# Kernel optimization log

Hardware: AMD Instinct MI355X
Metric: run time of the kernel (lower is better)

The kernel has to match this reference:

```python
import jax, jax.numpy as jnp
import numpy as np

DIM = 1024
DIM_HEAD = 64
HEADS = 16
NUM_LATENTS = 64
INNER = DIM_HEAD * HEADS  # 1024


def setup_inputs() -> dict:
    key = jax.random.key(0)
    ks = jax.random.split(key, 6)
    b, m, n = 8, 4, 1024
    x = jax.random.normal(ks[0], (b, m, n, DIM), dtype=jnp.float32)
    latents = jax.random.normal(ks[1], (NUM_LATENTS, DIM), dtype=jnp.float32)
    # Linear weights stored as (in, out); no bias for q/kv, bias for out (matches nn.Linear defaults)
    Wq = jax.random.normal(ks[2], (DIM, INNER), dtype=jnp.float32) * (DIM ** -0.5)
    Wkv = jax.random.normal(ks[3], (DIM, INNER * 2), dtype=jnp.float32) * (DIM ** -0.5)
    Wout = jax.random.normal(ks[4], (INNER, DIM), dtype=jnp.float32) * (INNER ** -0.5)
    bout = jax.random.normal(ks[5], (DIM,), dtype=jnp.float32) * 0.01
    return {"x": x, "latents": latents, "Wq": Wq, "Wkv": Wkv, "Wout": Wout, "bout": bout}


def reference(x, latents, Wq, Wkv, Wout, bout):
    b, m, n, d = x.shape
    h, dh = HEADS, DIM_HEAD
    scale = dh ** -0.5

    # q from latents: [n_lat, inner] -> [h, i, dh]
    q = (latents @ Wq).reshape(NUM_LATENTS, h, dh).transpose(1, 0, 2) * scale

    # k, v from media tokens: [b, m, n, 2*inner] -> two [b, h, m, n, dh]
    kv = x @ Wkv
    k, v = jnp.split(kv, 2, axis=-1)
    k = k.reshape(b, m, n, h, dh).transpose(0, 3, 1, 2, 4)  # b h m n dh
    v = v.reshape(b, m, n, h, dh).transpose(0, 3, 1, 2, 4)

    # latent k, v: [n_lat, 2*inner] -> [h, n_lat, dh] broadcast to [b, h, m, n_lat, dh]
    lkv = latents @ Wkv
    lk, lv = jnp.split(lkv, 2, axis=-1)
    lk = jnp.broadcast_to(lk.reshape(NUM_LATENTS, h, dh).transpose(1, 0, 2)[None, :, None], (b, h, m, NUM_LATENTS, dh))
    lv = jnp.broadcast_to(lv.reshape(NUM_LATENTS, h, dh).transpose(1, 0, 2)[None, :, None], (b, h, m, NUM_LATENTS, dh))

    k = jnp.concatenate((k, lk), axis=-2)  # b h m (n + n_lat) dh
    v = jnp.concatenate((v, lv), axis=-2)

    sim = jnp.einsum('hid,bhmjd->bhmij', q, k)
    attn = jax.nn.softmax(sim, axis=-1)  # stable softmax (max-subtract internal)
    out = jnp.einsum('bhmij,bhmjd->bhmid', attn, v)  # b h m i dh
    out = out.transpose(0, 2, 3, 1, 4).reshape(b, m, NUM_LATENTS, h * dh)  # b m i inner
    return out @ Wout + bout
```

## Files before the change

kernel.cpp:

```cpp
#include <hip/hip_runtime.h>
#include <cstdint>

typedef __attribute__((ext_vector_type(8))) __bf16 bf16x8;
typedef __attribute__((ext_vector_type(4))) float f32x4;
typedef __attribute__((ext_vector_type(8))) unsigned short u16x8;
typedef __attribute__((ext_vector_type(4))) unsigned short u16x4;

__device__ __forceinline__ unsigned short f2bf(float f) {
    union { float f; unsigned u; } v; v.f = f;
    unsigned u = v.u;
    return (unsigned short)((u + 0x7FFFu + ((u >> 16) & 1u)) >> 16);
}

__device__ __forceinline__ void gload_lds16(const void* g, void* l) {
    auto gp = reinterpret_cast<__attribute__((address_space(1))) unsigned*>(
        reinterpret_cast<uintptr_t>(g));
    auto lp = reinterpret_cast<__attribute__((address_space(3))) unsigned*>(
        reinterpret_cast<uintptr_t>(l));
    __builtin_amdgcn_global_load_lds(gp, lp, 16, 0, 0);
}

__global__ __launch_bounds__(256) void prep(const float* __restrict__ x,
                                            const float* __restrict__ latents,
                                            const float* __restrict__ Wq,
                                            const float* __restrict__ Wkv,
                                            const float* __restrict__ Wout,
                                            unsigned short* __restrict__ xb,
                                            unsigned short* __restrict__ latb,
                                            unsigned short* __restrict__ wqkvt,
                                            unsigned short* __restrict__ wkvt,
                                            unsigned short* __restrict__ woutt) {
    int b = blockIdx.x, tid = threadIdx.x;
    if (b < 2048) {
        int idx = b * 256 + tid, stride = 2048 * 256;
        for (int i = idx; i < 8388608; i += stride) {
            float4 v = ((const float4*)x)[i];
            u16x4 o;
            o.x = f2bf(v.x); o.y = f2bf(v.y); o.z = f2bf(v.z); o.w = f2bf(v.w);
            ((u16x4*)xb)[i] = o;
        }
        return;
    }
    b -= 2048;
    if (b < 64) {
        int i = b * 256 + tid;
        float4 v = ((const float4*)latents)[i];
        u16x4 o;
        o.x = f2bf(v.x); o.y = f2bf(v.y); o.z = f2bf(v.z); o.w = f2bf(v.w);
        ((u16x4*)latb)[i] = o;
        return;
    }
    b -= 64;
    const float* in; unsigned short* out; int R, C, bx, by;
    if (b < 1024)      { in = Wq;   out = wqkvt; R = 1024; C = 1024; bx = b & 31; by = b >> 5; }
    else if (b < 3072) { int v = b - 1024; in = Wkv;  out = wkvt;  R = 1024; C = 2048; bx = v & 63; by = v >> 6; }
    else               { int v = b - 3072; in = Wout; out = woutt; R = 1024; C = 1024; bx = v & 31; by = v >> 5; }
    __shared__ float t[32][33];
    int c0 = bx * 32, r0 = by * 32;
    int tx = tid & 31, ty = tid >> 5;
    for (int i = ty; i < 32; i += 8)
        t[i][tx] = in[(size_t)(r0 + i) * C + c0 + tx];
    __syncthreads();
    for (int i = ty; i < 32; i += 8)
        out[(size_t)(c0 + i) * R + r0 + tx] = f2bf(t[tx][i]);
}

__device__ __forceinline__ void gemm128p_body(const unsigned short* __restrict__ A,
                                              const unsigned short* __restrict__ Bt,
                                              void* __restrict__ C,
                                              const float* __restrict__ bias,
                                              unsigned short* __restrict__ vT,
                                              int M, int N, int K, float scale, int split,
                                              int c_f32, int vstart,
                                              int tid, int bid, int nwg,
                                              unsigned short* ldsbuf) {
#define LDSP(bi, half) (ldsbuf + ((bi) * 2 + (half)) * 4096)
    int ntx = N >> 7;
    int swz = bid;
    if ((nwg & 7) == 0) { int cpx = nwg >> 3; swz = (bid & 7) * cpx + (bid >> 3); }
    int m0 = (swz / ntx) << 7, n0 = (swz % ntx) << 7;
    int lane = tid & 63, w = tid >> 6;
    int wm = w >> 1, wn = w & 1;
    int lr = lane & 15, lg = lane >> 4;
    int gq = lg ^ ((lr >> 1) & 3);
    int nkt = K >> 5;

    int arow = tid >> 2;
    int sgl = (tid & 3) ^ ((arow >> 1) & 3);
    int ra0 = m0 + arow;      if (ra0 > M - 1) ra0 = M - 1;
    int ra1 = m0 + 64 + arow; if (ra1 > M - 1) ra1 = M - 1;
    const unsigned short* a0 = A + (size_t)ra0 * K + (sgl << 3);
    const unsigned short* a1 = A + (size_t)ra1 * K + (sgl << 3);
    const unsigned short* b0 = Bt + (size_t)(n0 + arow) * K + (sgl << 3);
    const unsigned short* b1 = Bt + (size_t)(n0 + 64 + arow) * K + (sgl << 3);

    f32x4 acc[4][4] = {};

#define ST_A128(bi, kt) do { \
        gload_lds16(a0 + ((kt) << 5), LDSP(bi, 0) + (w << 9)); \
        gload_lds16(a1 + ((kt) << 5), LDSP(bi, 0) + 2048 + (w << 9)); } while (0)
#define ST_B128(bi, kt) do { \
        gload_lds16(b0 + ((kt) << 5), LDSP(bi, 1) + (w << 9)); \
        gload_lds16(b1 + ((kt) << 5), LDSP(bi, 1) + 2048 + (w << 9)); } while (0)

    ST_A128(0, 0); ST_B128(0, 0);
    ST_A128(1, 1); ST_B128(1, 1);

    int buf = 0;
    for (int t = 0; t < nkt; ++t) {
        asm volatile("s_waitcnt vmcnt(4) lgkmcnt(0)" ::: "memory");
        __builtin_amdgcn_sched_barrier(0);
        __builtin_amdgcn_s_barrier();
        __builtin_amdgcn_sched_barrier(0);
        int st = t + 2; if (st >= nkt) st = nkt - 1;
        int sbuf = buf + 2; if (sbuf >= 3) sbuf -= 3;
        ST_A128(sbuf, st);
        ST_B128(sbuf, st);
        const unsigned short* pa = LDSP(buf, 0) + ((wm << 6) + lr) * 32 + (gq << 3);
        const unsigned short* pb = LDSP(buf, 1) + ((wn << 6) + lr) * 32 + (gq << 3);
        bf16x8 af[4], bfr[4];
#pragma unroll
        for (int nt = 0; nt < 4; nt++) bfr[nt] = *(const bf16x8*)(pb + nt * 512);
#pragma unroll
        for (int mt = 0; mt < 4; mt++) af[mt] = *(const bf16x8*)(pa + mt * 512);
        __builtin_amdgcn_s_setprio(1);
#pragma unroll
        for (int mt = 0; mt < 4; mt++)
#pragma unroll
            for (int nt = 0; nt < 4; nt++)
                acc[mt][nt] = __builtin_amdgcn_mfma_f32_16x16x32_bf16(af[mt], bfr[nt], acc[mt][nt], 0, 0, 0);
        __builtin_amdgcn_s_setprio(0);
        buf++; if (buf == 3) buf = 0;
    }
#undef ST_A128
#undef ST_B128
#undef LDSP

#pragma unroll
    for (int mt = 0; mt < 4; mt++) {
#pragma unroll
        for (int nt = 0; nt < 4; nt++) {
            int col = n0 + (wn << 6) + (nt << 4) + lr;
            float sc = (col < split) ? scale : 1.0f;
            float bv = bias ? bias[col] : 0.0f;
#pragma unroll
            for (int r = 0; r < 4; r++) {
                int row = m0 + (wm << 6) + (mt << 4) + (lg << 2) + r;
                if (row < M) {
                    float v = acc[mt][nt][r] * sc + bv;
                    if (vT && col >= vstart) vT[(size_t)(col - vstart) * 64 + row] = f2bf(v);
                    else if (c_f32) ((float*)C)[(size_t)row * N + col] = v;
                    else ((unsigned short*)C)[(size_t)row * N + col] = f2bf(v);
                }
            }
        }
    }
}

__global__ __launch_bounds__(256) void gemm128p(const unsigned short* __restrict__ A,
                                                const unsigned short* __restrict__ Bt,
                                                void* __restrict__ C,
                                                const float* __restrict__ bias,
                                                unsigned short* __restrict__ vT,
                                                int M, int N, int K, float scale, int split,
                                                int c_f32, int vstart) {
    __shared__ unsigned short lds[3 * 2 * 4096];
    gemm128p_body(A, Bt, C, bias, vT, M, N, K, scale, split, c_f32, vstart,
                  threadIdx.x, blockIdx.x, gridDim.x, lds);
}

__global__ __launch_bounds__(512, 2) void mega(const unsigned short* __restrict__ latb,
                                               const unsigned short* __restrict__ wqkvt,
                                               unsigned short* __restrict__ qlkvb,
                                               unsigned short* __restrict__ lvT,
                                               const unsigned short* __restrict__ A,
                                               const unsigned short* __restrict__ Bt,
                                               unsigned short* __restrict__ kb,
                                               unsigned short* __restrict__ vbT,
                                               int M, int N, int K) {
    __shared__ unsigned short lds[2][32768];

    if (blockIdx.x < 24) {
        gemm128p_body(latb, wqkvt, qlkvb, nullptr, lvT, 64, 3072, 1024, 0.125f, 1024, 0, 2048,
                      threadIdx.x & 255, blockIdx.x, 24, &lds[0][0]);
        return;
    }

    int nkt = K >> 6;
    int ntx = N >> 8;
    int nwg = (M >> 8) * (N >> 8);
    int bid = blockIdx.x - 24, swz = bid;
    if ((nwg & 7) == 0) { int cpx = nwg >> 3; swz = (bid & 7) * cpx + (bid >> 3); }
    int m0 = (swz / ntx) << 8, n0 = (swz % ntx) << 8;
    int tid = threadIdx.x, lane = tid & 63, w = tid >> 6;
    int wm = w >> 2, wn = w & 3;
    int lr = lane & 15, lg = lane >> 4;

    int srow = lane >> 3;
    int sg = (lane & 7) ^ srow;
    const unsigned short* aS = A + (size_t)(m0 + (w << 3) + srow) * K + (sg << 3);
    const unsigned short* bS = Bt + (size_t)(n0 + (w << 3) + srow) * K + (sg << 3);
    size_t rs64 = (size_t)64 * K;

    int baseA = (wm << 13) + lr * 64;
    int baseB = 16384 + (wn << 12) + lr * 64;
    int kg0 = (((0 << 2) + lg) ^ (lr & 7)) << 3;
    int kg1 = (((1 << 2) + lg) ^ (lr & 7)) << 3;

    f32x4 acc[8][4] = {};

#define ST_A(bi, kt) do { \
        gload_lds16(aS + ((size_t)(kt) << 6),          &lds[bi][(w << 9)]); \
        gload_lds16(aS + rs64 + ((size_t)(kt) << 6),   &lds[bi][4096 + (w << 9)]); \
        gload_lds16(aS + 2*rs64 + ((size_t)(kt) << 6), &lds[bi][8192 + (w << 9)]); \
        gload_lds16(aS + 3*rs64 + ((size_t)(kt) << 6), &lds[bi][12288 + (w << 9)]); } while (0)
#define ST_B(bi, kt) do { \
        gload_lds16(bS + ((size_t)(kt) << 6),          &lds[bi][16384 + (w << 9)]); \
        gload_lds16(bS + rs64 + ((size_t)(kt) << 6),   &lds[bi][20480 + (w << 9)]); \
        gload_lds16(bS + 2*rs64 + ((size_t)(kt) << 6), &lds[bi][24576 + (w << 9)]); \
        gload_lds16(bS + 3*rs64 + ((size_t)(kt) << 6), &lds[bi][28672 + (w << 9)]); } while (0)

    ST_A(0, 0);
    ST_B(0, 0);

    for (int t = 0; t < nkt; ++t) {
        int cur = t & 1, nxt = cur ^ 1;
        int st = t + 1; if (st >= nkt) st = nkt - 1;
        const unsigned short* L = &lds[cur][0];
        bf16x8 af[4], bfr[4];

        ST_A(nxt, st);
        __builtin_amdgcn_sched_barrier(0);
        asm volatile("s_waitcnt vmcnt(4)" ::: "memory");
        __builtin_amdgcn_sched_barrier(0);
        __builtin_amdgcn_s_barrier();
        __builtin_amdgcn_sched_barrier(0);
#pragma unroll
        for (int nt = 0; nt < 4; nt++) bfr[nt] = *(const bf16x8*)(L + baseB + nt * 1024 + kg0);
#pragma unroll
        for (int i = 0; i < 4; i++) af[i] = *(const bf16x8*)(L + baseA + i * 1024 + kg0);
        __builtin_amdgcn_s_setprio(1);
#pragma unroll
        for (int i = 0; i < 4; i++)
#pragma unroll
            for (int nt = 0; nt < 4; nt++)
                acc[i][nt] = __builtin_amdgcn_mfma_f32_16x16x32_bf16(af[i], bfr[nt], acc[i][nt], 0, 0, 0);
        __builtin_amdgcn_s_setprio(0);

        ST_B(nxt, st);
#pragma unroll
        for (int i = 0; i < 4; i++) af[i] = *(const bf16x8*)(L + baseA + (i + 4) * 1024 + kg0);
        __builtin_amdgcn_s_setprio(1);
#pragma unroll
        for (int i = 0; i < 4; i++)
#pragma unroll
            for (int nt = 0; nt < 4; nt++)
                acc[i + 4][nt] = __builtin_amdgcn_mfma_f32_16x16x32_bf16(af[i], bfr[nt], acc[i + 4][nt], 0, 0, 0);
        __builtin_amdgcn_s_setprio(0);

#pragma unroll
        for (int nt = 0; nt < 4; nt++) bfr[nt] = *(const bf16x8*)(L + baseB + nt * 1024 + kg1);
#pragma unroll
        for (int i = 0; i < 4; i++) af[i] = *(const bf16x8*)(L + baseA + i * 1024 + kg1);
        __builtin_amdgcn_s_setprio(1);
#pragma unroll
        for (int i = 0; i < 4; i++)
#pragma unroll
            for (int nt = 0; nt < 4; nt++)
                acc[i][nt] = __builtin_amdgcn_mfma_f32_16x16x32_bf16(af[i], bfr[nt], acc[i][nt], 0, 0, 0);
        __builtin_amdgcn_s_setprio(0);

#pragma unroll
        for (int i = 0; i < 4; i++) af[i] = *(const bf16x8*)(L + baseA + (i + 4) * 1024 + kg1);
        asm volatile("s_waitcnt lgkmcnt(0)" ::: "memory");
        __builtin_amdgcn_sched_barrier(0);
        __builtin_amdgcn_s_barrier();
        __builtin_amdgcn_sched_barrier(0);
        __builtin_amdgcn_s_setprio(1);
#pragma unroll
        for (int i = 0; i < 4; i++)
#pragma unroll
            for (int nt = 0; nt < 4; nt++)
                acc[i + 4][nt] = __builtin_amdgcn_mfma_f32_16x16x32_bf16(af[i], bfr[nt], acc[i + 4][nt], 0, 0, 0);
        __builtin_amdgcn_s_setprio(0);
    }
#undef ST_A
#undef ST_B

    if (n0 < 1024) {
#pragma unroll
        for (int mt = 0; mt < 8; mt++) {
#pragma unroll
            for (int nt = 0; nt < 4; nt++) {
                int col = n0 + (wn << 6) + (nt << 4) + lr;
                size_t rbase = (size_t)(m0 + (wm << 7) + (mt << 4) + (lg << 2));
#pragma unroll
                for (int r = 0; r < 4; r++)
                    kb[(rbase + r) * 1024 + col] = f2bf(acc[mt][nt][r]);
            }
        }
    } else {
#pragma unroll
        for (int mt = 0; mt < 8; mt++) {
#pragma unroll
            for (int nt = 0; nt < 4; nt++) {
                int dg = n0 - 1024 + (wn << 6) + (nt << 4) + lr;
                int rbase = m0 + (wm << 7) + (mt << 4) + (lg << 2);
                int bm = rbase >> 10, j = rbase & 1023;
                u16x4 o;
                o.x = f2bf(acc[mt][nt][0]); o.y = f2bf(acc[mt][nt][1]);
                o.z = f2bf(acc[mt][nt][2]); o.w = f2bf(acc[mt][nt][3]);
                *(u16x4*)(&vbT[((size_t)(bm << 10) + dg) * 1024 + j]) = o;
            }
        }
    }
}

__global__ __launch_bounds__(256) void attn_kernel(const unsigned short* __restrict__ qg, int qstride,
                                                   const unsigned short* __restrict__ kb,
                                                   const unsigned short* __restrict__ vbT,
                                                   const unsigned short* __restrict__ lkg, int lstride,
                                                   const unsigned short* __restrict__ lvT,
                                                   unsigned short* __restrict__ og) {
    __shared__ unsigned short K_lds[64 * 72];
    __shared__ unsigned short V_lds[64 * 72];
    __shared__ unsigned short P_lds[4][16 * 72];
    int bm = blockIdx.x >> 4, h = blockIdx.x & 15;
    int tid = threadIdx.x, lane = tid & 63, w = tid >> 6;
    int lr = lane & 15, lg = lane >> 4;

    bf16x8 qf[2];
#pragma unroll
    for (int kk = 0; kk < 2; kk++)
        qf[kk] = *(const bf16x8*)(qg + (size_t)((w << 4) + lr) * qstride + (h << 6) + (kk << 5) + (lg << 3));

    f32x4 acc[4] = {};
    float m_run[4], l_run[4];
#pragma unroll
    for (int r = 0; r < 4; r++) { m_run[r] = -1e30f; l_run[r] = 0.0f; }

    int jrow = tid >> 2;
    int seg = (tid & 3) << 4;

    const unsigned short* k_s = kb + (size_t)((bm << 10) + jrow) * 1024 + (h << 6) + seg;
    const unsigned short* v_s = vbT + (size_t)((bm << 10) + (h << 6) + jrow) * 1024 + seg;
    u16x8 k0 = *(const u16x8*)(k_s);
    u16x8 k1 = *(const u16x8*)(k_s + 8);
    u16x8 v0 = *(const u16x8*)(v_s);
    u16x8 v1 = *(const u16x8*)(v_s + 8);

    for (int t = 0; t < 17; t++) {
        *(u16x8*)(&K_lds[jrow * 72 + seg]) = k0;
        *(u16x8*)(&K_lds[jrow * 72 + seg + 8]) = k1;
        *(u16x8*)(&V_lds[jrow * 72 + seg]) = v0;
        *(u16x8*)(&V_lds[jrow * 72 + seg + 8]) = v1;
        __syncthreads();

        u16x8 nk0 = k0, nk1 = k1, nv0 = v0, nv1 = v1;
        if (t < 16) {
            if (t < 15) {
                const unsigned short* ks = kb + (size_t)((bm << 10) + ((t + 1) << 6) + jrow) * 1024 + (h << 6) + seg;
                const unsigned short* vs = vbT + (size_t)((bm << 10) + (h << 6) + jrow) * 1024 + ((t + 1) << 6) + seg;
                nk0 = *(const u16x8*)(ks);
                nk1 = *(const u16x8*)(ks + 8);
                nv0 = *(const u16x8*)(vs);
                nv1 = *(const u16x8*)(vs + 8);
            } else {
                const unsigned short* ks = lkg + (size_t)jrow * lstride + (h << 6) + seg;
                const unsigned short* vs = lvT + (size_t)((h << 6) + jrow) * 64 + seg;
                nk0 = *(const u16x8*)(ks);
                nk1 = *(const u16x8*)(ks + 8);
                nv0 = *(const u16x8*)(vs);
                nv1 = *(const u16x8*)(vs + 8);
            }
        }

        f32x4 s[4] = {};
#pragma unroll
        for (int jt = 0; jt < 4; jt++) {
#pragma unroll
            for (int kk = 0; kk < 2; kk++) {
                bf16x8 kf = *(const bf16x8*)(&K_lds[(size_t)((jt << 4) + lr) * 72 + (kk << 5) + (lg << 3)]);
                s[jt] = __builtin_amdgcn_mfma_f32_16x16x32_bf16(qf[kk], kf, s[jt], 0, 0, 0);
            }
        }
#pragma unroll
        for (int r = 0; r < 4; r++) {
            float mx = fmaxf(fmaxf(s[0][r], s[1][r]), fmaxf(s[2][r], s[3][r]));
            mx = fmaxf(mx, __shfl_xor(mx, 1));
            mx = fmaxf(mx, __shfl_xor(mx, 2));
            mx = fmaxf(mx, __shfl_xor(mx, 4));
            mx = fmaxf(mx, __shfl_xor(mx, 8));
            float nm = fmaxf(m_run[r], mx);
            float fct = __expf(m_run[r] - nm);
            m_run[r] = nm;
            float p0 = __expf(s[0][r] - nm);
            float p1 = __expf(s[1][r] - nm);
            float p2 = __expf(s[2][r] - nm);
            float p3 = __expf(s[3][r] - nm);
            float sum = p0 + p1 + p2 + p3;
            sum += __shfl_xor(sum, 1);
            sum += __shfl_xor(sum, 2);
            sum += __shfl_xor(sum, 4);
            sum += __shfl_xor(sum, 8);
            l_run[r] = l_run[r] * fct + sum;
#pragma unroll
            for (int dt = 0; dt < 4; dt++) acc[dt][r] *= fct;
            int prow = ((lg << 2) + r) * 72;
            P_lds[w][prow + lr]      = f2bf(p0);
            P_lds[w][prow + 16 + lr] = f2bf(p1);
            P_lds[w][prow + 32 + lr] = f2bf(p2);
            P_lds[w][prow + 48 + lr] = f2bf(p3);
        }
#pragma unroll
        for (int jkk = 0; jkk < 2; jkk++) {
            bf16x8 pf = *(const bf16x8*)(&P_lds[w][(size_t)lr * 72 + (jkk << 5) + (lg << 3)]);
#pragma unroll
            for (int dt = 0; dt < 4; dt++) {
                bf16x8 vf = *(const bf16x8*)(&V_lds[(size_t)((dt << 4) + lr) * 72 + (jkk << 5) + (lg << 3)]);
                acc[dt] = __builtin_amdgcn_mfma_f32_16x16x32_bf16(pf, vf, acc[dt], 0, 0, 0);
            }
        }
        __syncthreads();
        k0 = nk0; k1 = nk1; v0 = nv0; v1 = nv1;
    }
#pragma unroll
    for (int dt = 0; dt < 4; dt++) {
#pragma unroll
        for (int r = 0; r < 4; r++) {
            int i = (w << 4) + (lg << 2) + r;
            float v = acc[dt][r] / l_run[r];
            og[(size_t)((bm << 6) + i) * 1024 + (h << 6) + (dt << 4) + lr] = f2bf(v);
        }
    }
}

extern "C" void kernel_launch(void* const* d_in, const int* in_sizes, int n_in,
                              void* d_out, int out_size, void* d_ws, size_t ws_size,
                              hipStream_t stream) {
    const float* x       = (const float*)d_in[0];
    const float* latents = (const float*)d_in[1];
    const float* Wq      = (const float*)d_in[2];
    const float* Wkv     = (const float*)d_in[3];
    const float* Wout    = (const float*)d_in[4];
    const float* bout    = (const float*)d_in[5];
    char* ws = (char*)d_ws;
    unsigned short* xb    = (unsigned short*)(ws);
    unsigned short* kb    = (unsigned short*)(ws + 67108864);
    unsigned short* vbT   = (unsigned short*)(ws + 134217728);
    unsigned short* wqkvt = (unsigned short*)(ws + 201326592);
    unsigned short* wkvt  = wqkvt + 1024 * 1024;
    unsigned short* woutt = (unsigned short*)(ws + 207618048);
    unsigned short* latb  = (unsigned short*)(ws + 209715200);
    unsigned short* qlkvb = (unsigned short*)(ws + 209846272);
    unsigned short* attnb = (unsigned short*)(ws + 210239488);
    unsigned short* lvT   = (unsigned short*)(ws + 214433792);

    prep<<<6208, 256, 0, stream>>>(x, latents, Wq, Wkv, Wout, xb, latb, wqkvt, wkvt, woutt);
    mega<<<1048, 512, 0, stream>>>(latb, wqkvt, qlkvb, lvT, xb, wkvt, kb, vbT, 32768, 2048, 1024);
    attn_kernel<<<512, 256, 0, stream>>>(qlkvb, 3072, kb, vbT, qlkvb + 1024, 3072, lvT, attnb);
    gemm128p<<<128, 256, 0, stream>>>(attnb, woutt, (void*)d_out, bout, nullptr, 2048, 1024, 1024, 1.0f, 0, 1, 1 << 30);
}
```

Baseline: 241.0 us.

## Switch KV GEMM main loop to triple-buffered K=32 stages with prefetch depth two

Changes the large K/V projection GEMM in the mega kernel from a double-buffered pipeline with 64-wide K tiles to a triple-buffered pipeline with 32-wide K tiles, prefetching two stages ahead. LDS layout and swizzle are reworked for the narrower tile, and the global-to-LDS loads are redistributed so each thread issues one load per A/B half. The aim is to hide global load latency better while keeping total LDS per block the same. It doubles the number of loop iterations and adds several extra workgroup barriers per iteration, which could cost more than the deeper prefetch gains.

```diff
diff --git a/kernel.cpp b/kernel.cpp
--- a/kernel.cpp
+++ b/kernel.cpp
@@ -178,7 +178,7 @@
                                                unsigned short* __restrict__ kb,
                                                unsigned short* __restrict__ vbT,
                                                int M, int N, int K) {
-    __shared__ unsigned short lds[2][32768];
+    __shared__ unsigned short lds[3][16384];
 
     if (blockIdx.x < 24) {
         gemm128p_body(latb, wqkvt, qlkvb, nullptr, lvT, 64, 3072, 1024, 0.125f, 1024, 0, 2048,
@@ -186,7 +186,7 @@
         return;
     }
 
-    int nkt = K >> 6;
+    int nkt = K >> 5;
     int ntx = N >> 8;
     int nwg = (M >> 8) * (N >> 8);
     int bid = blockIdx.x - 24, swz = bid;
@@ -195,50 +195,48 @@
     int tid = threadIdx.x, lane = tid & 63, w = tid >> 6;
     int wm = w >> 2, wn = w & 3;
     int lr = lane & 15, lg = lane >> 4;
-
-    int srow = lane >> 3;
-    int sg = (lane & 7) ^ srow;
-    const unsigned short* aS = A + (size_t)(m0 + (w << 3) + srow) * K + (sg << 3);
-    const unsigned short* bS = Bt + (size_t)(n0 + (w << 3) + srow) * K + (sg << 3);
-    size_t rs64 = (size_t)64 * K;
-
-    int baseA = (wm << 13) + lr * 64;
-    int baseB = 16384 + (wn << 12) + lr * 64;
-    int kg0 = (((0 << 2) + lg) ^ (lr & 7)) << 3;
-    int kg1 = (((1 << 2) + lg) ^ (lr & 7)) << 3;
+    int gq = lg ^ ((lr >> 1) & 3);
+
+    int srow = tid >> 2;
+    int sgl = (tid & 3) ^ ((srow >> 1) & 3);
+    const unsigned short* a0 = A + (size_t)(m0 + srow) * K + (sgl << 3);
+    const unsigned short* a1 = A + (size_t)(m0 + 128 + srow) * K + (sgl << 3);
+    const unsigned short* b0 = Bt + (size_t)(n0 + srow) * K + (sgl << 3);
+    const unsigned short* b1 = Bt + (size_t)(n0 + 128 + srow) * K + (sgl << 3);
 
     f32x4 acc[8][4] = {};
 
-#define ST_A(bi, kt) do { \
-        gload_lds16(aS + ((size_t)(kt) << 6),          &lds[bi][(w << 9)]); \
-        gload_lds16(aS + rs64 + ((size_t)(kt) << 6),   &lds[bi][4096 + (w << 9)]); \
-        gload_lds16(aS + 2*rs64 + ((size_t)(kt) << 6), &lds[bi][8192 + (w << 9)]); \
-        gload_lds16(aS + 3*rs64 + ((size_t)(kt) << 6), &lds[bi][12288 + (w << 9)]); } while (0)
-#define ST_B(bi, kt) do { \
-        gload_lds16(bS + ((size_t)(kt) << 6),          &lds[bi][16384 + (w << 9)]); \
-        gload_lds16(bS + rs64 + ((size_t)(kt) << 6),   &lds[bi][20480 + (w << 9)]); \
-        gload_lds16(bS + 2*rs64 + ((size_t)(kt) << 6), &lds[bi][24576 + (w << 9)]); \
-        gload_lds16(bS + 3*rs64 + ((size_t)(kt) << 6), &lds[bi][28672 + (w << 9)]); } while (0)
-
-    ST_A(0, 0);
-    ST_B(0, 0);
-
+#define ST32(bi, kt) do { \
+        gload_lds16(a0 + ((kt) << 5), &lds[bi][w << 9]); \
+        gload_lds16(a1 + ((kt) << 5), &lds[bi][4096 + (w << 9)]); \
+        gload_lds16(b0 + ((kt) << 5), &lds[bi][8192 + (w << 9)]); \
+        gload_lds16(b1 + ((kt) << 5), &lds[bi][12288 + (w << 9)]); } while (0)
+
+    ST32(0, 0);
+    ST32(1, 1);
+    asm volatile("s_waitcnt vmcnt(4)" ::: "memory");
+    __builtin_amdgcn_s_barrier();
+    __builtin_amdgcn_sched_barrier(0);
+
+    int cur = 0;
     for (int t = 0; t < nkt; ++t) {
-        int cur = t & 1, nxt = cur ^ 1;
-        int st = t + 1; if (st >= nkt) st = nkt - 1;
-        const unsigned short* L = &lds[cur][0];
+        int st = t + 2; if (st >= nkt) st = nkt - 1;
+        int sbuf = cur + 2; if (sbuf >= 3) sbuf -= 3;
+
+        ST32(sbuf, st);
+        __builtin_amdgcn_sched_barrier(0);
+        asm volatile("s_waitcnt vmcnt(4)" ::: "memory");
+        __builtin_amdgcn_sched_barrier(0);
+        const unsigned short* pa = &lds[cur][((wm << 7) + lr) * 32 + (gq << 3)];
+        const unsigned short* pb = &lds[cur][8192 + ((wn << 6) + lr) * 32 + (gq << 3)];
         bf16x8 af[4], bfr[4];
-
-        ST_A(nxt, st);
-        __builtin_amdgcn_sched_barrier(0);
-        asm volatile("s_waitcnt vmcnt(4)" ::: "memory");
-        __builtin_amdgcn_sched_barrier(0);
+#pragma unroll
+        for (int nt = 0; nt < 4; nt++) bfr[nt] = *(const bf16x8*)(pb + nt * 512);
+#pragma unroll
+        for (int i = 0; i < 4; i++) af[i] = *(const bf16x8*)(pa + i * 512);
         __builtin_amdgcn_s_barrier();
-        __builtin_amdgcn_sched_barrier(0);
-#pragma unroll
-        for (int nt = 0; nt < 4; nt++) bfr[nt] = *(const bf16x8*)(L + baseB + nt * 1024 + kg0);
-#pragma unroll
-        for (int i = 0; i < 4; i++) af[i] = *(const bf16x8*)(L + baseA + i * 1024 + kg0);
+        asm volatile("s_waitcnt lgkmcnt(0)" ::: "memory");
+        __builtin_amdgcn_sched_barrier(0);
         __builtin_amdgcn_s_setprio(1);
 #pragma unroll
         for (int i = 0; i < 4; i++)
@@ -246,10 +244,13 @@
             for (int nt = 0; nt < 4; nt++)
                 acc[i][nt] = __builtin_amdgcn_mfma_f32_16x16x32_bf16(af[i], bfr[nt], acc[i][nt], 0, 0, 0);
         __builtin_amdgcn_s_setprio(0);
-
-        ST_B(nxt, st);
-#pragma unroll
-        for (int i = 0; i < 4; i++) af[i] = *(const bf16x8*)(L + baseA + (i + 4) * 1024 + kg0);
+        __builtin_amdgcn_s_barrier();
+
+#pragma unroll
+        for (int i = 0; i < 4; i++) af[i] = *(const bf16x8*)(pa + (i + 4) * 512);
+        __builtin_amdgcn_s_barrier();
+        asm volatile("s_waitcnt lgkmcnt(0)" ::: "memory");
+        __builtin_amdgcn_sched_barrier(0);
         __builtin_amdgcn_s_setprio(1);
 #pragma unroll
         for (int i = 0; i < 4; i++)
@@ -257,35 +258,12 @@
             for (int nt = 0; nt < 4; nt++)
                 acc[i + 4][nt] = __builtin_amdgcn_mfma_f32_16x16x32_bf16(af[i], bfr[nt], acc[i + 4][nt], 0, 0, 0);
         __builtin_amdgcn_s_setprio(0);
-
-#pragma unroll
-        for (int nt = 0; nt < 4; nt++) bfr[nt] = *(const bf16x8*)(L + baseB + nt * 1024 + kg1);
-#pragma unroll
-        for (int i = 0; i < 4; i++) af[i] = *(const bf16x8*)(L + baseA + i * 1024 + kg1);
-        __builtin_amdgcn_s_setprio(1);
-#pragma unroll
-        for (int i = 0; i < 4; i++)
-#pragma unroll
-            for (int nt = 0; nt < 4; nt++)
-                acc[i][nt] = __builtin_amdgcn_mfma_f32_16x16x32_bf16(af[i], bfr[nt], acc[i][nt], 0, 0, 0);
-        __builtin_amdgcn_s_setprio(0);
-
-#pragma unroll
-        for (int i = 0; i < 4; i++) af[i] = *(const bf16x8*)(L + baseA + (i + 4) * 1024 + kg1);
-        asm volatile("s_waitcnt lgkmcnt(0)" ::: "memory");
-        __builtin_amdgcn_sched_barrier(0);
         __builtin_amdgcn_s_barrier();
         __builtin_amdgcn_sched_barrier(0);
-        __builtin_amdgcn_s_setprio(1);
-#pragma unroll
-        for (int i = 0; i < 4; i++)
-#pragma unroll
-            for (int nt = 0; nt < 4; nt++)
-                acc[i + 4][nt] = __builtin_amdgcn_mfma_f32_16x16x32_bf16(af[i], bfr[nt], acc[i + 4][nt], 0, 0, 0);
-        __builtin_amdgcn_s_setprio(0);
-    }
-#undef ST_A
-#undef ST_B
+
+        cur++; if (cur == 3) cur = 0;
+    }
+#undef ST32
 
     if (n0 < 1024) {
 #pragma unroll
```

After: 261.2 us. 1.08x slower.

## Fold latent QKV projection into tail of big KV GEMM blocks

Applied to the files above, without the earlier changes.

Removes the 24 dedicated blocks in the fused kernel that computed the small latents×Wqkv projection with the 128-tile GEMM. Instead, the first 192 big-GEMM blocks each compute a 16-column slice of that projection after their main tile, split across 8 waves along K and reduced through LDS. The grid shrinks to exactly the big GEMM's tile count, which restores uniform swizzling and avoids the heterogeneous early blocks. The cost is extra tail work on some blocks, done with unstaged global loads.

```diff
diff --git a/kernel.cpp b/kernel.cpp
--- a/kernel.cpp
+++ b/kernel.cpp
@@ -65,21 +65,18 @@
         out[(size_t)(c0 + i) * R + r0 + tx] = f2bf(t[tx][i]);
 }
 
-__device__ __forceinline__ void gemm128p_body(const unsigned short* __restrict__ A,
-                                              const unsigned short* __restrict__ Bt,
-                                              void* __restrict__ C,
-                                              const float* __restrict__ bias,
-                                              unsigned short* __restrict__ vT,
-                                              int M, int N, int K, float scale, int split,
-                                              int c_f32, int vstart,
-                                              int tid, int bid, int nwg,
-                                              unsigned short* ldsbuf) {
-#define LDSP(bi, half) (ldsbuf + ((bi) * 2 + (half)) * 4096)
+__global__ __launch_bounds__(256) void gemm128p(const unsigned short* __restrict__ A,
+                                                const unsigned short* __restrict__ Bt,
+                                                void* __restrict__ C,
+                                                const float* __restrict__ bias,
+                                                int M, int N, int K, float scale, int split,
+                                                int c_f32) {
+    __shared__ unsigned short lds[3][2][4096];
     int ntx = N >> 7;
-    int swz = bid;
+    int nwg = gridDim.x, bid = blockIdx.x, swz = bid;
     if ((nwg & 7) == 0) { int cpx = nwg >> 3; swz = (bid & 7) * cpx + (bid >> 3); }
     int m0 = (swz / ntx) << 7, n0 = (swz % ntx) << 7;
-    int lane = tid & 63, w = tid >> 6;
+    int tid = threadIdx.x, lane = tid & 63, w = tid >> 6;
     int wm = w >> 1, wn = w & 1;
     int lr = lane & 15, lg = lane >> 4;
     int gq = lg ^ ((lr >> 1) & 3);
@@ -97,11 +94,11 @@
     f32x4 acc[4][4] = {};
 
 #define ST_A128(bi, kt) do { \
-        gload_lds16(a0 + ((kt) << 5), LDSP(bi, 0) + (w << 9)); \
-        gload_lds16(a1 + ((kt) << 5), LDSP(bi, 0) + 2048 + (w << 9)); } while (0)
+        gload_lds16(a0 + ((kt) << 5), &lds[bi][0][w << 9]); \
+        gload_lds16(a1 + ((kt) << 5), &lds[bi][0][2048 + (w << 9)]); } while (0)
 #define ST_B128(bi, kt) do { \
-        gload_lds16(b0 + ((kt) << 5), LDSP(bi, 1) + (w << 9)); \
-        gload_lds16(b1 + ((kt) << 5), LDSP(bi, 1) + 2048 + (w << 9)); } while (0)
+        gload_lds16(b0 + ((kt) << 5), &lds[bi][1][w << 9]); \
+        gload_lds16(b1 + ((kt) << 5), &lds[bi][1][2048 + (w << 9)]); } while (0)
 
     ST_A128(0, 0); ST_B128(0, 0);
     ST_A128(1, 1); ST_B128(1, 1);
@@ -116,8 +113,8 @@
         int sbuf = buf + 2; if (sbuf >= 3) sbuf -= 3;
         ST_A128(sbuf, st);
         ST_B128(sbuf, st);
-        const unsigned short* pa = LDSP(buf, 0) + ((wm << 6) + lr) * 32 + (gq << 3);
-        const unsigned short* pb = LDSP(buf, 1) + ((wn << 6) + lr) * 32 + (gq << 3);
+        const unsigned short* pa = &lds[buf][0][((wm << 6) + lr) * 32 + (gq << 3)];
+        const unsigned short* pb = &lds[buf][1][((wn << 6) + lr) * 32 + (gq << 3)];
         bf16x8 af[4], bfr[4];
 #pragma unroll
         for (int nt = 0; nt < 4; nt++) bfr[nt] = *(const bf16x8*)(pb + nt * 512);
@@ -134,7 +131,6 @@
     }
 #undef ST_A128
 #undef ST_B128
-#undef LDSP
 
 #pragma unroll
     for (int mt = 0; mt < 4; mt++) {
@@ -148,25 +144,12 @@
                 int row = m0 + (wm << 6) + (mt << 4) + (lg << 2) + r;
                 if (row < M) {
                     float v = acc[mt][nt][r] * sc + bv;
-                    if (vT && col >= vstart) vT[(size_t)(col - vstart) * 64 + row] = f2bf(v);
-                    else if (c_f32) ((float*)C)[(size_t)row * N + col] = v;
-                    else ((unsigned short*)C)[(size_t)row * N + col] = f2bf(v);
+                    if (c_f32) ((float*)C)[(size_t)row * N + col] = v;
+                    else       ((unsigned short*)C)[(size_t)row * N + col] = f2bf(v);
                 }
             }
         }
     }
-}
-
-__global__ __launch_bounds__(256) void gemm128p(const unsigned short* __restrict__ A,
-                                                const unsigned short* __restrict__ Bt,
-                                                void* __restrict__ C,
-                                                const float* __restrict__ bias,
-                                                unsigned short* __restrict__ vT,
-                                                int M, int N, int K, float scale, int split,
-                                                int c_f32, int vstart) {
-    __shared__ unsigned short lds[3 * 2 * 4096];
-    gemm128p_body(A, Bt, C, bias, vT, M, N, K, scale, split, c_f32, vstart,
-                  threadIdx.x, blockIdx.x, gridDim.x, lds);
 }
 
 __global__ __launch_bounds__(512, 2) void mega(const unsigned short* __restrict__ latb,
@@ -178,18 +161,12 @@
                                                unsigned short* __restrict__ kb,
                                                unsigned short* __restrict__ vbT,
                                                int M, int N, int K) {
-    __shared__ unsigned short lds[2][32768];
-
-    if (blockIdx.x < 24) {
-        gemm128p_body(latb, wqkvt, qlkvb, nullptr, lvT, 64, 3072, 1024, 0.125f, 1024, 0, 2048,
-                      threadIdx.x & 255, blockIdx.x, 24, &lds[0][0]);
-        return;
-    }
+    __shared__ __attribute__((aligned(16))) unsigned short lds[2][32768];
 
     int nkt = K >> 6;
     int ntx = N >> 8;
-    int nwg = (M >> 8) * (N >> 8);
-    int bid = blockIdx.x - 24, swz = bid;
+    int nwg = gridDim.x;
+    int bid = blockIdx.x, swz = bid;
     if ((nwg & 7) == 0) { int cpx = nwg >> 3; swz = (bid & 7) * cpx + (bid >> 3); }
     int m0 = (swz / ntx) << 8, n0 = (swz % ntx) << 8;
     int tid = threadIdx.x, lane = tid & 63, w = tid >> 6;
@@ -311,6 +288,42 @@
                 o.x = f2bf(acc[mt][nt][0]); o.y = f2bf(acc[mt][nt][1]);
                 o.z = f2bf(acc[mt][nt][2]); o.w = f2bf(acc[mt][nt][3]);
                 *(u16x4*)(&vbT[((size_t)(bm << 10) + dg) * 1024 + j]) = o;
+            }
+        }
+    }
+
+    if (bid < 192) {
+        int col0 = bid << 4;
+        f32x4 qa[4] = {};
+        int kbase = w << 7;
+#pragma unroll
+        for (int ks = 0; ks < 4; ks++) {
+            int k = kbase + (ks << 5) + (lg << 3);
+            bf16x8 bf = *(const bf16x8*)(wqkvt + (size_t)(col0 + lr) * 1024 + k);
+#pragma unroll
+            for (int mt = 0; mt < 4; mt++) {
+                bf16x8 afr = *(const bf16x8*)(latb + (size_t)((mt << 4) + lr) * 1024 + k);
+                qa[mt] = __builtin_amdgcn_mfma_f32_16x16x32_bf16(afr, bf, qa[mt], 0, 0, 0);
+            }
+        }
+        asm volatile("s_waitcnt vmcnt(0)" ::: "memory");
+        __builtin_amdgcn_s_barrier();
+        f32x4* red = (f32x4*)&lds[0][0];
+#pragma unroll
+        for (int mt = 0; mt < 4; mt++) red[((w << 2) + mt) * 64 + lane] = qa[mt];
+        __syncthreads();
+        if (w < 4) {
+            f32x4 s = red[(w) * 64 + lane];
+#pragma unroll
+            for (int ww = 1; ww < 8; ww++) s += red[((ww << 2) + w) * 64 + lane];
+            int col = col0 + lr;
+            float sc = (col < 1024) ? 0.125f : 1.0f;
+#pragma unroll
+            for (int r = 0; r < 4; r++) {
+                int row = (w << 4) + (lg << 2) + r;
+                float v = s[r] * sc;
+                if (col >= 2048) lvT[(size_t)(col - 2048) * 64 + row] = f2bf(v);
+                else             qlkvb[(size_t)row * 3072 + col] = f2bf(v);
             }
         }
     }
@@ -457,7 +470,7 @@
     unsigned short* lvT   = (unsigned short*)(ws + 214433792);
 
     prep<<<6208, 256, 0, stream>>>(x, latents, Wq, Wkv, Wout, xb, latb, wqkvt, wkvt, woutt);
-    mega<<<1048, 512, 0, stream>>>(latb, wqkvt, qlkvb, lvT, xb, wkvt, kb, vbT, 32768, 2048, 1024);
+    mega<<<1024, 512, 0, stream>>>(latb, wqkvt, qlkvb, lvT, xb, wkvt, kb, vbT, 32768, 2048, 1024);
     attn_kernel<<<512, 256, 0, stream>>>(qlkvb, 3072, kb, vbT, qlkvb + 1024, 3072, lvT, attnb);
-    gemm128p<<<128, 256, 0, stream>>>(attnb, woutt, (void*)d_out, bout, nullptr, 2048, 1024, 1024, 1.0f, 0, 1, 1 << 30);
-}
+    gemm128p<<<128, 256, 0, stream>>>(attnb, woutt, (void*)d_out, bout, 2048, 1024, 1024, 1.0f, 0, 1);
+}
```

After: 229.1 us. -4.9%, faster.
